# Kernel tuning notes

Hardware: AMD Instinct MI355X
Metric: run time of the kernel (lower is better)

The kernel has to match this reference:

```python
import jax, jax.numpy as jnp
import numpy as np

IN_DIM = 256
OUT_DIM = 256

def setup_inputs() -> dict:
    key = jax.random.key(0)
    k1, k2, k3, k4 = jax.random.split(key, 4)
    B, N, K, D = 4, 10000, 16, IN_DIM
    x = jax.random.normal(k1, (B, N, D), dtype=jnp.float32)
    neigh = jax.random.randint(k2, (N, K), 0, N, dtype=jnp.int64)
    # nn.Linear(2*in_dim, out_dim): W [out, 2*in], b [out]
    bound = 1.0 / np.sqrt(2 * D)
    W = jax.random.uniform(k3, (OUT_DIM, 2 * D), minval=-bound, maxval=bound, dtype=jnp.float32)
    b = jax.random.uniform(k4, (OUT_DIM,), minval=-bound, maxval=bound, dtype=jnp.float32)
    return {"x": x, "neigh": neigh, "W": W, "b": b}

def reference(x, neigh, W, b):
    # x: [B,N,D], neigh: [N,K] with -1 = padding
    mask = (neigh >= 0)                                # [N,K]
    idx = jnp.clip(neigh, 0, None)                     # [N,K]
    # batch_gather_nodes: x_nei[b,n,k,:] = x[b, idx[n,k], :]
    x_nei = x[:, idx, :]                               # [B,N,K,D]
    x_nei = x_nei * mask[None, :, :, None].astype(x.dtype)
    denom = jnp.clip(mask.sum(axis=1), 1, None).astype(x.dtype)  # [N]
    agg = x_nei.sum(axis=2) / denom[None, :, None]     # [B,N,D]
    h = jnp.concatenate([x, agg], axis=-1)             # [B,N,2D]
    return jax.nn.relu(jnp.einsum('bnd,od->bno', h, W) + b)
```

## Files before the change

kernel.cpp:

```cpp
#include <hip/hip_runtime.h>
#include <hip/hip_bf16.h>
#include <stdint.h>

#define B_   4
#define N_   10000
#define K_   16
#define D_   256
#define OUT_ 256
#define KDIM 512
#define M_   (B_ * N_)

typedef __attribute__((ext_vector_type(8))) short  short8;
typedef __attribute__((ext_vector_type(4))) float  f32x4;
typedef __attribute__((ext_vector_type(4))) unsigned short ushort4_t;

__device__ inline unsigned short f2bf(float f) {
    __hip_bfloat16 h = __float2bfloat16(f);
    return *reinterpret_cast<unsigned short*>(&h);
}
__device__ inline float bf2f(unsigned short u) {
    unsigned int v = ((unsigned int)u) << 16;
    return __builtin_bit_cast(float, v);
}

__global__ __launch_bounds__(256) void xprep(const float* __restrict__ x,
                                             unsigned short* __restrict__ h,
                                             unsigned short* __restrict__ xg) {
    const int n    = blockIdx.x;
    const int b    = threadIdx.x >> 6;
    const int lane = threadIdx.x & 63;

    float4 v = ((const float4*)x)[(size_t)(b * N_ + n) * 64 + lane];
    ushort4_t s;
    s.x = f2bf(v.x); s.y = f2bf(v.y); s.z = f2bf(v.z); s.w = f2bf(v.w);

    *(ushort4_t*)(h  + ((size_t)b * N_ + n) * KDIM + lane * 4) = s;
    *(ushort4_t*)(xg + ((size_t)n * B_ + b) * D_   + lane * 4) = s;
}

__global__ __launch_bounds__(256) void agg_build2(const unsigned short* __restrict__ xg,
                                                  const int*            __restrict__ neigh,
                                                  unsigned short*       __restrict__ h) {
    const int n    = blockIdx.x;
    const int tid  = threadIdx.x;
    const int b    = tid >> 6;
    const int lane = tid & 63;

    __shared__ int idx_s[K_];
    if (tid < K_) idx_s[tid] = neigh[n * K_ + tid];
    __syncthreads();

    int cnt = 0;
#pragma unroll
    for (int k = 0; k < K_; ++k) cnt += (idx_s[k] >= 0) ? 1 : 0;
    const float inv = 1.0f / (float)(cnt > 1 ? cnt : 1);

    float ax = 0.f, ay = 0.f, az = 0.f, aw = 0.f;
#pragma unroll
    for (int k = 0; k < K_; ++k) {
        int j = idx_s[k];
        if (j >= 0) {
            ushort4_t v = *(const ushort4_t*)(xg + ((size_t)j * B_ + b) * D_ + lane * 4);
            ax += bf2f(v.x); ay += bf2f(v.y); az += bf2f(v.z); aw += bf2f(v.w);
        }
    }

    ushort4_t s;
    s.x = f2bf(ax * inv); s.y = f2bf(ay * inv);
    s.z = f2bf(az * inv); s.w = f2bf(aw * inv);
    *(ushort4_t*)(h + ((size_t)b * N_ + n) * KDIM + D_ + lane * 4) = s;
}

__global__ __launch_bounds__(256) void wconv(const float* __restrict__ W,
                                             unsigned short* __restrict__ Wb) {
    int g = blockIdx.x * 256 + threadIdx.x;
    float4 v = ((const float4*)W)[g];
    ushort4_t s;
    s.x = f2bf(v.x); s.y = f2bf(v.y); s.z = f2bf(v.z); s.w = f2bf(v.w);
    ((ushort4_t*)Wb)[g] = s;
}

__global__ __launch_bounds__(256) void gemm_bt2(const unsigned short* __restrict__ A,
                                                const unsigned short* __restrict__ Bm,
                                                const float* __restrict__ bias,
                                                float* __restrict__ out) {
    __shared__ unsigned short As[64 * 32];
    __shared__ unsigned short Bs[256 * 32];

    const int tid    = threadIdx.x;
    const int w      = tid >> 6;
    const int lane   = tid & 63;
    const int tile_m = blockIdx.x * 64;
    const int q      = lane >> 4;
    const int r16    = lane & 15;

    f32x4 acc[4][4] = {};

    const int crow = lane >> 2;
    const int kofs = (lane & 3) * 8;

    for (int kk = 0; kk < KDIM; kk += 32) {
#pragma unroll
        for (int t = 0; t < 5; ++t) {
            const int c = w * 5 + t;
            if (c < 4) {
                const int row = c * 16 + crow;
                const unsigned short* ga = A + (size_t)(tile_m + row) * KDIM + kk + kofs;
                __builtin_amdgcn_global_load_lds(
                    (const __attribute__((address_space(1))) void*)ga,
                    (__attribute__((address_space(3))) void*)(As + c * 512),
                    16, 0, 0);
            } else {
                const int row = (c - 4) * 16 + crow;
                const unsigned short* gb = Bm + (size_t)row * KDIM + kk + kofs;
                __builtin_amdgcn_global_load_lds(
                    (const __attribute__((address_space(1))) void*)gb,
                    (__attribute__((address_space(3))) void*)(Bs + (c - 4) * 512),
                    16, 0, 0);
            }
        }
        __syncthreads();

        short8 a[4], bf[4];
#pragma unroll
        for (int i = 0; i < 4; ++i)
            a[i] = *(const short8*)(As + (i * 16 + r16) * 32 + q * 8);
#pragma unroll
        for (int j = 0; j < 4; ++j)
            bf[j] = *(const short8*)(Bs + (w * 64 + j * 16 + r16) * 32 + q * 8);

#pragma unroll
        for (int i = 0; i < 4; ++i)
#pragma unroll
            for (int j = 0; j < 4; ++j)
                acc[i][j] = __builtin_amdgcn_mfma_f32_16x16x32_bf16(a[i], bf[j], acc[i][j], 0, 0, 0);

        __syncthreads();
    }

    float bj[4];
#pragma unroll
    for (int j = 0; j < 4; ++j)
        bj[j] = bias[w * 64 + j * 16 + r16];

#pragma unroll
    for (int i = 0; i < 4; ++i) {
#pragma unroll
        for (int reg = 0; reg < 4; ++reg) {
            const int m = tile_m + i * 16 + q * 4 + reg;
            float* orow = out + (size_t)m * OUT_ + w * 64;
#pragma unroll
            for (int j = 0; j < 4; ++j) {
                float v = acc[i][j][reg] + bj[j];
                orow[j * 16 + r16] = v > 0.f ? v : 0.f;
            }
        }
    }
}

extern "C" void kernel_launch(void* const* d_in, const int* in_sizes, int n_in,
                              void* d_out, int out_size, void* d_ws, size_t ws_size,
                              hipStream_t stream) {
    const float* x     = (const float*)d_in[0];
    const int*   neigh = (const int*)d_in[1];
    const float* W     = (const float*)d_in[2];
    const float* bias  = (const float*)d_in[3];
    float*       out   = (float*)d_out;

    unsigned short* Wb = (unsigned short*)d_ws;
    unsigned short* h  = Wb + OUT_ * KDIM;
    unsigned short* xg = h + (size_t)M_ * KDIM;

    xprep<<<N_, 256, 0, stream>>>(x, h, xg);
    wconv<<<128, 256, 0, stream>>>(W, Wb);
    agg_build2<<<N_, 256, 0, stream>>>(xg, neigh, h);
    gemm_bt2<<<M_ / 64, 256, 0, stream>>>(h, Wb, bias, out);
}
```

Baseline: 162.2 us.

## Fuse neighbor aggregation into GEMM, building A tile in LDS directly

Merges the aggregation kernel into the GEMM. Each block gathers and averages neighbor features for 16 nodes across all 4 batches straight into a full-K LDS tile, then runs the MFMA loop over that tile with W fragments read directly from global memory. This drops the intermediate h buffer (its write and re-read) and one kernel launch. xprep now writes only the node-major xg layout, using wider 8-element stores. In exchange, B fragments are no longer staged in LDS, the LDS footprint grows to about 66 KB, and the gather uses masked unconditional loads instead of branches.

Result: faster. 158.6 us (-2.3%).

```diff
diff --git a/kernel.cpp b/kernel.cpp
--- a/kernel.cpp
+++ b/kernel.cpp
@@ -10,8 +10,11 @@
 #define KDIM 512
 #define M_   (B_ * N_)
 
-typedef __attribute__((ext_vector_type(8))) short  short8;
-typedef __attribute__((ext_vector_type(4))) float  f32x4;
+#define CH_STRIDE 2056
+
+typedef __attribute__((ext_vector_type(8))) short          short8;
+typedef __attribute__((ext_vector_type(8))) unsigned short ushort8;
+typedef __attribute__((ext_vector_type(4))) float          f32x4;
 typedef __attribute__((ext_vector_type(4))) unsigned short ushort4_t;
 
 __device__ inline unsigned short f2bf(float f) {
@@ -23,52 +26,20 @@
     return __builtin_bit_cast(float, v);
 }
 
-__global__ __launch_bounds__(256) void xprep(const float* __restrict__ x,
-                                             unsigned short* __restrict__ h,
-                                             unsigned short* __restrict__ xg) {
-    const int n    = blockIdx.x;
-    const int b    = threadIdx.x >> 6;
-    const int lane = threadIdx.x & 63;
+__global__ __launch_bounds__(256) void xprep2(const float* __restrict__ x,
+                                              unsigned short* __restrict__ xg) {
+    const int t  = threadIdx.x;
+    const int n  = blockIdx.x * 2 + (t >> 7);
+    const int b  = (t >> 5) & 3;
+    const int c0 = (t & 31) * 8;
 
-    float4 v = ((const float4*)x)[(size_t)(b * N_ + n) * 64 + lane];
-    ushort4_t s;
-    s.x = f2bf(v.x); s.y = f2bf(v.y); s.z = f2bf(v.z); s.w = f2bf(v.w);
-
-    *(ushort4_t*)(h  + ((size_t)b * N_ + n) * KDIM + lane * 4) = s;
-    *(ushort4_t*)(xg + ((size_t)n * B_ + b) * D_   + lane * 4) = s;
-}
-
-__global__ __launch_bounds__(256) void agg_build2(const unsigned short* __restrict__ xg,
-                                                  const int*            __restrict__ neigh,
-                                                  unsigned short*       __restrict__ h) {
-    const int n    = blockIdx.x;
-    const int tid  = threadIdx.x;
-    const int b    = tid >> 6;
-    const int lane = tid & 63;
-
-    __shared__ int idx_s[K_];
-    if (tid < K_) idx_s[tid] = neigh[n * K_ + tid];
-    __syncthreads();
-
-    int cnt = 0;
-#pragma unroll
-    for (int k = 0; k < K_; ++k) cnt += (idx_s[k] >= 0) ? 1 : 0;
-    const float inv = 1.0f / (float)(cnt > 1 ? cnt : 1);
-
-    float ax = 0.f, ay = 0.f, az = 0.f, aw = 0.f;
-#pragma unroll
-    for (int k = 0; k < K_; ++k) {
-        int j = idx_s[k];
-        if (j >= 0) {
-            ushort4_t v = *(const ushort4_t*)(xg + ((size_t)j * B_ + b) * D_ + lane * 4);
-            ax += bf2f(v.x); ay += bf2f(v.y); az += bf2f(v.z); aw += bf2f(v.w);
-        }
-    }
-
-    ushort4_t s;
-    s.x = f2bf(ax * inv); s.y = f2bf(ay * inv);
-    s.z = f2bf(az * inv); s.w = f2bf(aw * inv);
-    *(ushort4_t*)(h + ((size_t)b * N_ + n) * KDIM + D_ + lane * 4) = s;
+    const float4* xr = (const float4*)(x + ((size_t)b * N_ + n) * D_ + c0);
+    float4 v0 = xr[0];
+    float4 v1 = xr[1];
+    ushort8 s;
+    s[0] = f2bf(v0.x); s[1] = f2bf(v0.y); s[2] = f2bf(v0.z); s[3] = f2bf(v0.w);
+    s[4] = f2bf(v1.x); s[5] = f2bf(v1.y); s[6] = f2bf(v1.z); s[7] = f2bf(v1.w);
+    *(ushort8*)(xg + ((size_t)n * B_ + b) * D_ + c0) = s;
 }
 
 __global__ __launch_bounds__(256) void wconv(const float* __restrict__ W,
@@ -80,62 +51,76 @@
     ((ushort4_t*)Wb)[g] = s;
 }
 
-__global__ __launch_bounds__(256) void gemm_bt2(const unsigned short* __restrict__ A,
-                                                const unsigned short* __restrict__ Bm,
-                                                const float* __restrict__ bias,
-                                                float* __restrict__ out) {
-    __shared__ unsigned short As[64 * 32];
-    __shared__ unsigned short Bs[256 * 32];
+__global__ __launch_bounds__(256) void fused_gemm(const unsigned short* __restrict__ xg,
+                                                  const int*            __restrict__ neigh,
+                                                  const unsigned short* __restrict__ Bm,
+                                                  const float*          __restrict__ bias,
+                                                  float*                __restrict__ out) {
+    __shared__ unsigned short As[16 * CH_STRIDE];
+    __shared__ int idx_s[256];
 
-    const int tid    = threadIdx.x;
-    const int w      = tid >> 6;
-    const int lane   = tid & 63;
-    const int tile_m = blockIdx.x * 64;
-    const int q      = lane >> 4;
-    const int r16    = lane & 15;
+    const int tid = threadIdx.x;
+    const int n0  = blockIdx.x * 16;
 
-    f32x4 acc[4][4] = {};
+    idx_s[tid] = neigh[n0 * K_ + tid];
+    __syncthreads();
 
-    const int crow = lane >> 2;
-    const int kofs = (lane & 3) * 8;
+    const int grp = tid >> 5;
+    const int gl  = tid & 31;
+    const int ch  = gl >> 2;
+    const int off = (gl & 3) * 8;
 
-    for (int kk = 0; kk < KDIM; kk += 32) {
+    for (int t = 0; t < 8; ++t) {
+        const int ar   = grp * 8 + t;
+        const int node = ar >> 2;
+        const int b    = ar & 3;
+
+        float acc[8] = {0.f, 0.f, 0.f, 0.f, 0.f, 0.f, 0.f, 0.f};
+        int cnt = 0;
 #pragma unroll
-        for (int t = 0; t < 5; ++t) {
-            const int c = w * 5 + t;
-            if (c < 4) {
-                const int row = c * 16 + crow;
-                const unsigned short* ga = A + (size_t)(tile_m + row) * KDIM + kk + kofs;
-                __builtin_amdgcn_global_load_lds(
-                    (const __attribute__((address_space(1))) void*)ga,
-                    (__attribute__((address_space(3))) void*)(As + c * 512),
-                    16, 0, 0);
-            } else {
-                const int row = (c - 4) * 16 + crow;
-                const unsigned short* gb = Bm + (size_t)row * KDIM + kk + kofs;
-                __builtin_amdgcn_global_load_lds(
-                    (const __attribute__((address_space(1))) void*)gb,
-                    (__attribute__((address_space(3))) void*)(Bs + (c - 4) * 512),
-                    16, 0, 0);
-            }
+        for (int k = 0; k < K_; ++k) {
+            const int j   = idx_s[node * K_ + k];
+            const int jc  = j >= 0 ? j : 0;
+            const float m = j >= 0 ? 1.f : 0.f;
+            cnt += j >= 0 ? 1 : 0;
+            ushort8 v = *(const ushort8*)(xg + (((size_t)jc * B_ + b) << 8) + gl * 8);
+#pragma unroll
+            for (int e = 0; e < 8; ++e) acc[e] += bf2f(v[e]) * m;
         }
-        __syncthreads();
+        const float inv = 1.0f / (float)(cnt > 1 ? cnt : 1);
 
+        ushort8 s;
+#pragma unroll
+        for (int e = 0; e < 8; ++e) s[e] = f2bf(acc[e] * inv);
+        *(ushort8*)(As + (8 + ch) * CH_STRIDE + ar * 32 + off) = s;
+
+        ushort8 sv = *(const ushort8*)(xg + (((size_t)(n0 + node) * B_ + b) << 8) + gl * 8);
+        *(ushort8*)(As + ch * CH_STRIDE + ar * 32 + off) = sv;
+    }
+    __syncthreads();
+
+    const int w    = tid >> 6;
+    const int lane = tid & 63;
+    const int q    = lane >> 4;
+    const int r16  = lane & 15;
+
+    f32x4 acc2[4][4] = {};
+
+#pragma unroll 4
+    for (int c = 0; c < 16; ++c) {
         short8 a[4], bf[4];
 #pragma unroll
         for (int i = 0; i < 4; ++i)
-            a[i] = *(const short8*)(As + (i * 16 + r16) * 32 + q * 8);
+            a[i] = *(const short8*)(As + c * CH_STRIDE + (i * 16 + r16) * 32 + q * 8);
 #pragma unroll
         for (int j = 0; j < 4; ++j)
-            bf[j] = *(const short8*)(Bs + (w * 64 + j * 16 + r16) * 32 + q * 8);
+            bf[j] = *(const short8*)(Bm + (size_t)(w * 64 + j * 16 + r16) * KDIM + c * 32 + q * 8);
 
 #pragma unroll
         for (int i = 0; i < 4; ++i)
 #pragma unroll
             for (int j = 0; j < 4; ++j)
-                acc[i][j] = __builtin_amdgcn_mfma_f32_16x16x32_bf16(a[i], bf[j], acc[i][j], 0, 0, 0);
-
-        __syncthreads();
+                acc2[i][j] = __builtin_amdgcn_mfma_f32_16x16x32_bf16(a[i], bf[j], acc2[i][j], 0, 0, 0);
     }
 
     float bj[4];
@@ -147,11 +132,12 @@
     for (int i = 0; i < 4; ++i) {
 #pragma unroll
         for (int reg = 0; reg < 4; ++reg) {
-            const int m = tile_m + i * 16 + q * 4 + reg;
-            float* orow = out + (size_t)m * OUT_ + w * 64;
+            const int ar = i * 16 + q * 4 + reg;
+            const size_t m = (size_t)(ar & 3) * N_ + n0 + (ar >> 2);
+            float* orow = out + m * OUT_ + w * 64;
 #pragma unroll
             for (int j = 0; j < 4; ++j) {
-                float v = acc[i][j][reg] + bj[j];
+                float v = acc2[i][j][reg] + bj[j];
                 orow[j * 16 + r16] = v > 0.f ? v : 0.f;
             }
         }
@@ -168,11 +154,9 @@
     float*       out   = (float*)d_out;
 
     unsigned short* Wb = (unsigned short*)d_ws;
-    unsigned short* h  = Wb + OUT_ * KDIM;
-    unsigned short* xg = h + (size_t)M_ * KDIM;
+    unsigned short* xg = Wb + OUT_ * KDIM;
 
-    xprep<<<N_, 256, 0, stream>>>(x, h, xg);
+    xprep2<<<N_ / 2, 256, 0, stream>>>(x, xg);
     wconv<<<128, 256, 0, stream>>>(W, Wb);
-    agg_build2<<<N_, 256, 0, stream>>>(xg, neigh, h);
-    gemm_bt2<<<M_ / 64, 256, 0, stream>>>(h, Wb, bias, out);
+    fused_gemm<<<N_ / 16, 256, 0, stream>>>(xg, neigh, Wb, bias, out);
 }
```

## Chunk bf16 gather buffer by feature columns and merge prep kernels

Applied to the files above, without the earlier changes.

The intermediate bf16 copy of x is relaid into 8 column chunks of 32 features ([chunk][node][batch][32]), so each gather block touches only one chunk and the gathered neighbour rows are more likely to stay resident in cache. The aggregation kernel now handles 8 nodes per block, issues all 16 neighbour loads before summing, and masks padding with a multiply instead of a branch. The x conversion and W conversion kernels are merged into one launch with wider 8-element stores. The trade-off is smaller 8-byte gather loads per thread and extra index bookkeeping.

Result: faster. 140.6 us (-13.4%).

```diff
diff --git a/kernel.cpp b/kernel.cpp
--- a/kernel.cpp
+++ b/kernel.cpp
@@ -9,9 +9,12 @@
 #define OUT_ 256
 #define KDIM 512
 #define M_   (B_ * N_)
-
-typedef __attribute__((ext_vector_type(8))) short  short8;
-typedef __attribute__((ext_vector_type(4))) float  f32x4;
+#define CW   32
+#define NCH  8
+
+typedef __attribute__((ext_vector_type(8))) short          short8;
+typedef __attribute__((ext_vector_type(8))) unsigned short ushort8;
+typedef __attribute__((ext_vector_type(4))) float          f32x4;
 typedef __attribute__((ext_vector_type(4))) unsigned short ushort4_t;
 
 __device__ inline unsigned short f2bf(float f) {
@@ -23,61 +26,89 @@
     return __builtin_bit_cast(float, v);
 }
 
-__global__ __launch_bounds__(256) void xprep(const float* __restrict__ x,
-                                             unsigned short* __restrict__ h,
-                                             unsigned short* __restrict__ xg) {
-    const int n    = blockIdx.x;
-    const int b    = threadIdx.x >> 6;
-    const int lane = threadIdx.x & 63;
-
-    float4 v = ((const float4*)x)[(size_t)(b * N_ + n) * 64 + lane];
-    ushort4_t s;
-    s.x = f2bf(v.x); s.y = f2bf(v.y); s.z = f2bf(v.z); s.w = f2bf(v.w);
-
-    *(ushort4_t*)(h  + ((size_t)b * N_ + n) * KDIM + lane * 4) = s;
-    *(ushort4_t*)(xg + ((size_t)n * B_ + b) * D_   + lane * 4) = s;
-}
-
-__global__ __launch_bounds__(256) void agg_build2(const unsigned short* __restrict__ xg,
+__global__ __launch_bounds__(256) void prep(const float* __restrict__ x,
+                                            const float* __restrict__ W,
+                                            unsigned short* __restrict__ h,
+                                            unsigned short* __restrict__ xc,
+                                            unsigned short* __restrict__ Wb) {
+    const int t = threadIdx.x;
+    if (blockIdx.x < 5000) {
+        const int n  = blockIdx.x * 2 + (t >> 7);
+        const int b  = (t >> 5) & 3;
+        const int c0 = (t & 31) * 8;
+        const float4* xr = (const float4*)(x + ((size_t)b * N_ + n) * D_ + c0);
+        float4 v0 = xr[0];
+        float4 v1 = xr[1];
+        ushort8 s;
+        s[0] = f2bf(v0.x); s[1] = f2bf(v0.y); s[2] = f2bf(v0.z); s[3] = f2bf(v0.w);
+        s[4] = f2bf(v1.x); s[5] = f2bf(v1.y); s[6] = f2bf(v1.z); s[7] = f2bf(v1.w);
+        *(ushort8*)(h + ((size_t)b * N_ + n) * KDIM + c0) = s;
+        const int ch  = c0 >> 5;
+        const int col = c0 & 31;
+        *(ushort8*)(xc + (((size_t)ch * N_ + n) * B_ + b) * CW + col) = s;
+    } else {
+        int g = (blockIdx.x - 5000) * 256 + t;
+        float4 v = ((const float4*)W)[g];
+        ushort4_t s;
+        s.x = f2bf(v.x); s.y = f2bf(v.y); s.z = f2bf(v.z); s.w = f2bf(v.w);
+        ((ushort4_t*)Wb)[g] = s;
+    }
+}
+
+__global__ __launch_bounds__(256) void gather_agg(const unsigned short* __restrict__ xc,
                                                   const int*            __restrict__ neigh,
                                                   unsigned short*       __restrict__ h) {
-    const int n    = blockIdx.x;
-    const int tid  = threadIdx.x;
-    const int b    = tid >> 6;
-    const int lane = tid & 63;
-
-    __shared__ int idx_s[K_];
-    if (tid < K_) idx_s[tid] = neigh[n * K_ + tid];
+    const int c   = blockIdx.x & 7;
+    const int g   = blockIdx.x >> 3;
+    const int n0  = g * 8;
+    const int tid = threadIdx.x;
+
+    __shared__ int   idx_s[8 * K_];
+    __shared__ float inv_s[8];
+
+    if (tid < 8 * K_) idx_s[tid] = neigh[n0 * K_ + tid];
     __syncthreads();
-
-    int cnt = 0;
-#pragma unroll
-    for (int k = 0; k < K_; ++k) cnt += (idx_s[k] >= 0) ? 1 : 0;
-    const float inv = 1.0f / (float)(cnt > 1 ? cnt : 1);
-
-    float ax = 0.f, ay = 0.f, az = 0.f, aw = 0.f;
+    if (tid < 8) {
+        int cnt = 0;
+#pragma unroll
+        for (int k = 0; k < K_; ++k) cnt += idx_s[tid * K_ + k] >= 0 ? 1 : 0;
+        inv_s[tid] = 1.0f / (float)(cnt > 1 ? cnt : 1);
+    }
+    __syncthreads();
+
+    const int q  = tid & 7;
+    const int tl = tid >> 3;
+    const int ns = tl >> 2;
+    const int b  = tl & 3;
+
+    const unsigned short* xcc = xc + (size_t)c * N_ * B_ * CW;
+
+    int jj[K_];
+#pragma unroll
+    for (int k = 0; k < K_; ++k) jj[k] = idx_s[ns * K_ + k];
+
+    ushort4_t vv[K_];
 #pragma unroll
     for (int k = 0; k < K_; ++k) {
-        int j = idx_s[k];
-        if (j >= 0) {
-            ushort4_t v = *(const ushort4_t*)(xg + ((size_t)j * B_ + b) * D_ + lane * 4);
-            ax += bf2f(v.x); ay += bf2f(v.y); az += bf2f(v.z); aw += bf2f(v.w);
-        }
-    }
+        const int jc = jj[k] >= 0 ? jj[k] : 0;
+        vv[k] = *(const ushort4_t*)(xcc + ((size_t)jc * B_ + b) * CW + q * 4);
+    }
+
+    float a0 = 0.f, a1 = 0.f, a2 = 0.f, a3 = 0.f;
+#pragma unroll
+    for (int k = 0; k < K_; ++k) {
+        const float m = jj[k] >= 0 ? 1.f : 0.f;
+        a0 += bf2f(vv[k].x) * m;
+        a1 += bf2f(vv[k].y) * m;
+        a2 += bf2f(vv[k].z) * m;
+        a3 += bf2f(vv[k].w) * m;
+    }
+    const float inv = inv_s[ns];
 
     ushort4_t s;
-    s.x = f2bf(ax * inv); s.y = f2bf(ay * inv);
-    s.z = f2bf(az * inv); s.w = f2bf(aw * inv);
-    *(ushort4_t*)(h + ((size_t)b * N_ + n) * KDIM + D_ + lane * 4) = s;
-}
-
-__global__ __launch_bounds__(256) void wconv(const float* __restrict__ W,
-                                             unsigned short* __restrict__ Wb) {
-    int g = blockIdx.x * 256 + threadIdx.x;
-    float4 v = ((const float4*)W)[g];
-    ushort4_t s;
-    s.x = f2bf(v.x); s.y = f2bf(v.y); s.z = f2bf(v.z); s.w = f2bf(v.w);
-    ((ushort4_t*)Wb)[g] = s;
+    s.x = f2bf(a0 * inv); s.y = f2bf(a1 * inv);
+    s.z = f2bf(a2 * inv); s.w = f2bf(a3 * inv);
+    *(ushort4_t*)(h + ((size_t)b * N_ + n0 + ns) * KDIM + D_ + c * CW + q * 4) = s;
 }
 
 __global__ __launch_bounds__(256) void gemm_bt2(const unsigned short* __restrict__ A,
@@ -169,10 +200,9 @@
 
     unsigned short* Wb = (unsigned short*)d_ws;
     unsigned short* h  = Wb + OUT_ * KDIM;
-    unsigned short* xg = h + (size_t)M_ * KDIM;
-
-    xprep<<<N_, 256, 0, stream>>>(x, h, xg);
-    wconv<<<128, 256, 0, stream>>>(W, Wb);
-    agg_build2<<<N_, 256, 0, stream>>>(xg, neigh, h);
+    unsigned short* xc = h + (size_t)M_ * KDIM;
+
+    prep<<<5000 + 128, 256, 0, stream>>>(x, W, h, xc, Wb);
+    gather_agg<<<(N_ / 8) * NCH, 256, 0, stream>>>(xc, neigh, h);
     gemm_bt2<<<M_ / 64, 256, 0, stream>>>(h, Wb, bias, out);
 }
```
